# Optimization experiments

Measured on AMD Instinct MI355X. Metric: run time of the kernel, lower is better.

Reference implementation:

```python
import jax, jax.numpy as jnp
import numpy as np

N_NODES = 100000
N_EDGES = 1600000
D = 128
LN_EPS = 1e-5


def setup_inputs() -> dict:
    key = jax.random.key(0)
    ks = jax.random.split(key, 6)
    return {
        "x": jax.random.normal(ks[0], (N_NODES, D), dtype=jnp.float32),
        "edge_src": jax.random.randint(ks[1], (N_EDGES,), 0, N_NODES, dtype=jnp.int32),
        "edge_dst": jax.random.randint(ks[2], (N_EDGES,), 0, N_NODES, dtype=jnp.int32),
        "edge_val": jax.random.uniform(ks[3], (N_EDGES,), dtype=jnp.float32),
        "w1": jax.random.normal(ks[4], (D,), dtype=jnp.float32),
        "w2": jax.random.normal(ks[5], (D,), dtype=jnp.float32),
        "ln1_g": jnp.ones((D,), dtype=jnp.float32),
        "ln1_b": jnp.zeros((D,), dtype=jnp.float32),
        "ln2_g": jnp.ones((D,), dtype=jnp.float32),
        "ln2_b": jnp.zeros((D,), dtype=jnp.float32),
    }


def _layer_norm(x, g, b):
    mu = jnp.mean(x, axis=-1, keepdims=True)
    var = jnp.mean(jnp.square(x - mu), axis=-1, keepdims=True)
    return (x - mu) * jax.lax.rsqrt(var + LN_EPS) * g + b


def _gat_layer(x, w, src, dst, val, g, b):
    # diag transform: h = x * w  (elementwise over features)
    h = x * w
    # sparse adjacency aggregation: out[dst] += val * h[src]
    msg = val[:, None] * h[src]  # [E, D]
    out = jax.ops.segment_sum(msg, dst, num_segments=x.shape[0])
    return _layer_norm(out, g, b)


def reference(x, edge_src, edge_dst, edge_val, w1, w2, ln1_g, ln1_b, ln2_g, ln2_b):
    # layer 0 (followed by ReLU; dropout is identity in eval mode)
    h = _gat_layer(x, w1, edge_src, edge_dst, edge_val, ln1_g, ln1_b)
    h = jax.nn.relu(h)
    # layer 1 (last layer: no ReLU/dropout)
    out = _gat_layer(h, w2, edge_src, edge_dst, edge_val, ln2_g, ln2_b)
    return out
```

## Files before the change

### kernel.cpp

```cpp
#include <hip/hip_runtime.h>

typedef __fp16 half2_t __attribute__((ext_vector_type(2)));

#define D 128
#define LN_EPS 1e-5f
#define BUCKET_NODES 128
#define BUCKET_SHIFT 7
#define EDGE_CAP 4096
#define FUSE_THREADS 512
#define K2_EPT 32
#define GT 1024

__device__ inline unsigned pack_h2(float a, float b) {
    half2_t p = __builtin_amdgcn_cvt_pkrtz(a, b);
    return __builtin_bit_cast(unsigned, p);
}

__global__ __launch_bounds__(FUSE_THREADS)
void conv_fill_kernel(const float* __restrict__ x, unsigned int* __restrict__ xb,
                      int conv_items, int conv_blocks,
                      const int* __restrict__ src, const int* __restrict__ dst,
                      const float* __restrict__ val,
                      int* __restrict__ gcnt, uint2* __restrict__ edges,
                      int E, int nbuckets) {
    if ((int)blockIdx.x < conv_blocks) {
        int i4 = blockIdx.x * FUSE_THREADS + threadIdx.x;
        if (i4 < conv_items) {
            int node = i4 >> 4, f4 = (i4 & 15) << 2;
            float4 xA = *(const float4*)(x + (size_t)node * D + f4);
            float4 xB = *(const float4*)(x + (size_t)node * D + 64 + f4);
            uint4 pw;
            pw.x = pack_h2(xA.x, xB.x); pw.y = pack_h2(xA.y, xB.y);
            pw.z = pack_h2(xA.z, xB.z); pw.w = pack_h2(xA.w, xB.w);
            *(uint4*)(xb + (size_t)node * 64 + f4) = pw;
        }
        return;
    }
    __shared__ int lcnt[1024];
    __shared__ int lbase[1024];
    int fb = (int)blockIdx.x - conv_blocks;
    for (int i = threadIdx.x; i < nbuckets; i += FUSE_THREADS) lcnt[i] = 0;
    __syncthreads();

    int base = fb * (FUSE_THREADS * K2_EPT);
    unsigned int br[K2_EPT];
    #pragma unroll
    for (int r = 0; r < K2_EPT; ++r) {
        int e = base + r * FUSE_THREADS + threadIdx.x;
        if (e < E) {
            int d = dst[e];
            int b = d >> BUCKET_SHIFT;
            int rk = atomicAdd(&lcnt[b], 1);
            br[r] = ((unsigned)b << 21) | ((unsigned)(d & (BUCKET_NODES - 1)) << 14)
                  | (unsigned)rk;
        }
    }
    __syncthreads();
    for (int i = threadIdx.x; i < nbuckets; i += FUSE_THREADS) {
        int c = lcnt[i];
        lbase[i] = c ? atomicAdd(&gcnt[i], c) : 0;
    }
    __syncthreads();
    #pragma unroll
    for (int r = 0; r < K2_EPT; ++r) {
        int e = base + r * FUSE_THREADS + threadIdx.x;
        if (e < E) {
            unsigned u = br[r];
            int b    = (int)(u >> 21);
            int dstl = (int)((u >> 14) & 127u);
            int rk   = (int)(u & 16383u);
            int slot = lbase[b] + rk;
            if (slot < EDGE_CAP)
                edges[(size_t)b * EDGE_CAP + slot] =
                    make_uint2((unsigned)src[e] | ((unsigned)dstl << 20),
                               __float_as_uint(val[e]));
        }
    }
}

__global__ __launch_bounds__(GT, 8)
void gather_ln_kernel(const uint4* __restrict__ h4,
                      const int* __restrict__ gcnt,
                      const uint2* __restrict__ edges_g,
                      const float* __restrict__ w,
                      const float* __restrict__ g,
                      const float* __restrict__ bb,
                      float* __restrict__ out_f32,
                      unsigned int* __restrict__ out_h,
                      int N, int mode) {
    __shared__ uint2 eL[EDGE_CAP];
    __shared__ int hist[BUCKET_NODES];
    __shared__ int scanb[BUCKET_NODES];
    __shared__ int obase[BUCKET_NODES];

    int bkt = blockIdx.x;
    int tid = threadIdx.x;
    int cnt = min(gcnt[bkt], EDGE_CAP);
    const uint2* ep = edges_g + (size_t)bkt * EDGE_CAP;

    if (tid < BUCKET_NODES) hist[tid] = 0;
    __syncthreads();

    uint2 ed[4]; int dl[4]; int rk[4];
    #pragma unroll
    for (int r = 0; r < 4; ++r) {
        int i = r * GT + tid;
        if (i < cnt) {
            uint2 t = ep[i];
            ed[r] = t;
            dl[r] = (int)(t.x >> 20);
            rk[r] = atomicAdd(&hist[dl[r]], 1);
        } else dl[r] = -1;
    }
    __syncthreads();
    if (tid < BUCKET_NODES) scanb[tid] = hist[tid];
    __syncthreads();
    #pragma unroll
    for (int off = 1; off < BUCKET_NODES; off <<= 1) {
        int v = 0;
        if (tid < BUCKET_NODES && tid >= off) v = scanb[tid - off];
        __syncthreads();
        if (tid < BUCKET_NODES) scanb[tid] += v;
        __syncthreads();
    }
    if (tid < BUCKET_NODES) obase[tid] = scanb[tid] - hist[tid];
    __syncthreads();
    #pragma unroll
    for (int r = 0; r < 4; ++r)
        if (dl[r] >= 0) eL[obase[dl[r]] + rk[r]] = ed[r];
    __syncthreads();

    int wid = tid >> 6, lane = tid & 63, grp = lane >> 4, sl = lane & 15;

    float4 wA = ((const float4*)w)[sl];
    float4 wB = ((const float4*)(w + 64))[sl];
    float4 gA = ((const float4*)g)[sl];
    float4 gB = ((const float4*)(g + 64))[sl];
    float4 bA = ((const float4*)bb)[sl];
    float4 bB = ((const float4*)(bb + 64))[sl];

    #pragma unroll
    for (int k = 0; k < 2; ++k) {
        int ni = k * 64 + wid * 4 + grp;
        int n = (bkt << BUCKET_SHIFT) + ni;
        if (n >= N) continue;
        int st = obase[ni], m = hist[ni];

        float aA0=0,aA1=0,aA2=0,aA3=0, aB0=0,aB1=0,aB2=0,aB3=0;
        for (int j = 0; j < m; j += 2) {
            uint2 tA = eL[st + j];
            uint2 tB = (j + 1 < m) ? eL[st + j + 1] : make_uint2(0u, 0u);
            int   sA = (int)(tA.x & 0xfffffu);
            float vA = __uint_as_float(tA.y);
            int   sB = (int)(tB.x & 0xfffffu);
            float vB = __uint_as_float(tB.y);
            uint4 hA = h4[(size_t)sA * 16 + sl];
            uint4 hB = h4[(size_t)sB * 16 + sl];
            half2_t p;
            p = __builtin_bit_cast(half2_t, hA.x);
            aA0 = fmaf(vA, (float)p.x, aA0); aB0 = fmaf(vA, (float)p.y, aB0);
            p = __builtin_bit_cast(half2_t, hA.y);
            aA1 = fmaf(vA, (float)p.x, aA1); aB1 = fmaf(vA, (float)p.y, aB1);
            p = __builtin_bit_cast(half2_t, hA.z);
            aA2 = fmaf(vA, (float)p.x, aA2); aB2 = fmaf(vA, (float)p.y, aB2);
            p = __builtin_bit_cast(half2_t, hA.w);
            aA3 = fmaf(vA, (float)p.x, aA3); aB3 = fmaf(vA, (float)p.y, aB3);
            p = __builtin_bit_cast(half2_t, hB.x);
            aA0 = fmaf(vB, (float)p.x, aA0); aB0 = fmaf(vB, (float)p.y, aB0);
            p = __builtin_bit_cast(half2_t, hB.y);
            aA1 = fmaf(vB, (float)p.x, aA1); aB1 = fmaf(vB, (float)p.y, aB1);
            p = __builtin_bit_cast(half2_t, hB.z);
            aA2 = fmaf(vB, (float)p.x, aA2); aB2 = fmaf(vB, (float)p.y, aB2);
            p = __builtin_bit_cast(half2_t, hB.w);
            aA3 = fmaf(vB, (float)p.x, aA3); aB3 = fmaf(vB, (float)p.y, aB3);
        }

        aA0 *= wA.x; aA1 *= wA.y; aA2 *= wA.z; aA3 *= wA.w;
        aB0 *= wB.x; aB1 *= wB.y; aB2 *= wB.z; aB3 *= wB.w;

        float sum = ((aA0 + aA1) + (aA2 + aA3)) + ((aB0 + aB1) + (aB2 + aB3));
        sum += __shfl_xor(sum, 1, 64); sum += __shfl_xor(sum, 2, 64);
        sum += __shfl_xor(sum, 4, 64); sum += __shfl_xor(sum, 8, 64);
        float mu = sum * (1.0f / D);

        float dA0 = aA0 - mu, dA1 = aA1 - mu, dA2 = aA2 - mu, dA3 = aA3 - mu;
        float dB0 = aB0 - mu, dB1 = aB1 - mu, dB2 = aB2 - mu, dB3 = aB3 - mu;
        float sq = ((dA0*dA0 + dA1*dA1) + (dA2*dA2 + dA3*dA3))
                 + ((dB0*dB0 + dB1*dB1) + (dB2*dB2 + dB3*dB3));
        sq += __shfl_xor(sq, 1, 64); sq += __shfl_xor(sq, 2, 64);
        sq += __shfl_xor(sq, 4, 64); sq += __shfl_xor(sq, 8, 64);
        float rstd = rsqrtf(sq * (1.0f / D) + LN_EPS);

        float oA0 = dA0 * rstd * gA.x + bA.x, oA1 = dA1 * rstd * gA.y + bA.y;
        float oA2 = dA2 * rstd * gA.z + bA.z, oA3 = dA3 * rstd * gA.w + bA.w;
        float oB0 = dB0 * rstd * gB.x + bB.x, oB1 = dB1 * rstd * gB.y + bB.y;
        float oB2 = dB2 * rstd * gB.z + bB.z, oB3 = dB3 * rstd * gB.w + bB.w;

        if (mode == 1) {
            oA0 = fmaxf(oA0, 0.f); oA1 = fmaxf(oA1, 0.f);
            oA2 = fmaxf(oA2, 0.f); oA3 = fmaxf(oA3, 0.f);
            oB0 = fmaxf(oB0, 0.f); oB1 = fmaxf(oB1, 0.f);
            oB2 = fmaxf(oB2, 0.f); oB3 = fmaxf(oB3, 0.f);
            uint4 pw;
            pw.x = pack_h2(oA0, oB0); pw.y = pack_h2(oA1, oB1);
            pw.z = pack_h2(oA2, oB2); pw.w = pack_h2(oA3, oB3);
            ((uint4*)(out_h + (size_t)n * 64))[sl] = pw;
        } else {
            ((float4*)(out_f32 + (size_t)n * D))[sl]      = make_float4(oA0, oA1, oA2, oA3);
            ((float4*)(out_f32 + (size_t)n * D + 64))[sl] = make_float4(oB0, oB1, oB2, oB3);
        }
    }
}

extern "C" void kernel_launch(void* const* d_in, const int* in_sizes, int n_in,
                              void* d_out, int out_size, void* d_ws, size_t ws_size,
                              hipStream_t stream) {
    const float* x    = (const float*)d_in[0];
    const int*   esrc = (const int*)d_in[1];
    const int*   edst = (const int*)d_in[2];
    const float* eval_= (const float*)d_in[3];
    const float* w1   = (const float*)d_in[4];
    const float* w2   = (const float*)d_in[5];
    const float* g1   = (const float*)d_in[6];
    const float* b1   = (const float*)d_in[7];
    const float* g2   = (const float*)d_in[8];
    const float* b2   = (const float*)d_in[9];
    float* out = (float*)d_out;

    const int N = in_sizes[0] / D;
    const int E = in_sizes[1];
    const int nbuckets = (N + BUCKET_NODES - 1) >> BUCKET_SHIFT;

    unsigned int* xb    = (unsigned int*)d_ws;
    unsigned int* hb    = xb + (size_t)N * 64;
    uint2*        edges = (uint2*)(hb + (size_t)N * 64);
    int*          gcnt  = (int*)(edges + (size_t)nbuckets * EDGE_CAP);

    const int conv_items  = N * 16;
    const int conv_blocks = (conv_items + FUSE_THREADS - 1) / FUSE_THREADS;
    const int fill_blocks = (E + FUSE_THREADS * K2_EPT - 1) / (FUSE_THREADS * K2_EPT);

    (void)hipMemsetAsync(gcnt, 0, (size_t)nbuckets * sizeof(int), stream);
    conv_fill_kernel<<<conv_blocks + fill_blocks, FUSE_THREADS, 0, stream>>>(
        x, xb, conv_items, conv_blocks, esrc, edst, eval_, gcnt, edges, E, nbuckets);
    gather_ln_kernel<<<nbuckets, GT, 0, stream>>>((const uint4*)xb, gcnt, edges,
                                                  w1, g1, b1, nullptr, hb, N, 1);
    gather_ln_kernel<<<nbuckets, GT, 0, stream>>>((const uint4*)hb, gcnt, edges,
                                                  w2, g2, b2, out, nullptr, N, 0);
}
```

Before: 333.2 us.

## Split edge fill into more blocks and keep edge payload in registers

Cuts edges handled per thread in the bucketing fill from 32 to 4, launching many more fill blocks and placing them ahead of the fp16 conversion blocks. The src/val payload is loaded once during the counting pass and held in registers instead of being re-read after the global offset reservation. This raises parallelism and reduces the long serial per-block latency, at the cost of many more per-bucket global atomics on the shared counter array.

```diff
diff --git a/kernel.cpp b/kernel.cpp
--- a/kernel.cpp
+++ b/kernel.cpp
@@ -8,7 +8,7 @@
 #define BUCKET_SHIFT 7
 #define EDGE_CAP 4096
 #define FUSE_THREADS 512
-#define K2_EPT 32
+#define K2_EPT 4
 #define GT 1024
 
 __device__ inline unsigned pack_h2(float a, float b) {
@@ -18,13 +18,13 @@
 
 __global__ __launch_bounds__(FUSE_THREADS)
 void conv_fill_kernel(const float* __restrict__ x, unsigned int* __restrict__ xb,
-                      int conv_items, int conv_blocks,
+                      int conv_items, int fill_blocks,
                       const int* __restrict__ src, const int* __restrict__ dst,
                       const float* __restrict__ val,
                       int* __restrict__ gcnt, uint2* __restrict__ edges,
                       int E, int nbuckets) {
-    if ((int)blockIdx.x < conv_blocks) {
-        int i4 = blockIdx.x * FUSE_THREADS + threadIdx.x;
+    if ((int)blockIdx.x >= fill_blocks) {
+        int i4 = ((int)blockIdx.x - fill_blocks) * FUSE_THREADS + threadIdx.x;
         if (i4 < conv_items) {
             int node = i4 >> 4, f4 = (i4 & 15) << 2;
             float4 xA = *(const float4*)(x + (size_t)node * D + f4);
@@ -38,12 +38,14 @@
     }
     __shared__ int lcnt[1024];
     __shared__ int lbase[1024];
-    int fb = (int)blockIdx.x - conv_blocks;
+    int fb = (int)blockIdx.x;
     for (int i = threadIdx.x; i < nbuckets; i += FUSE_THREADS) lcnt[i] = 0;
     __syncthreads();
 
     int base = fb * (FUSE_THREADS * K2_EPT);
-    unsigned int br[K2_EPT];
+    unsigned int w0[K2_EPT];
+    float        w1[K2_EPT];
+    int          br[K2_EPT];
     #pragma unroll
     for (int r = 0; r < K2_EPT; ++r) {
         int e = base + r * FUSE_THREADS + threadIdx.x;
@@ -51,8 +53,11 @@
             int d = dst[e];
             int b = d >> BUCKET_SHIFT;
             int rk = atomicAdd(&lcnt[b], 1);
-            br[r] = ((unsigned)b << 21) | ((unsigned)(d & (BUCKET_NODES - 1)) << 14)
-                  | (unsigned)rk;
+            w0[r] = (unsigned)src[e] | ((unsigned)(d & (BUCKET_NODES - 1)) << 20);
+            w1[r] = val[e];
+            br[r] = (b << 16) | rk;
+        } else {
+            br[r] = -1;
         }
     }
     __syncthreads();
@@ -63,17 +68,13 @@
     __syncthreads();
     #pragma unroll
     for (int r = 0; r < K2_EPT; ++r) {
-        int e = base + r * FUSE_THREADS + threadIdx.x;
-        if (e < E) {
-            unsigned u = br[r];
-            int b    = (int)(u >> 21);
-            int dstl = (int)((u >> 14) & 127u);
-            int rk   = (int)(u & 16383u);
+        if (br[r] >= 0) {
+            int b    = br[r] >> 16;
+            int rk   = br[r] & 0xffff;
             int slot = lbase[b] + rk;
             if (slot < EDGE_CAP)
                 edges[(size_t)b * EDGE_CAP + slot] =
-                    make_uint2((unsigned)src[e] | ((unsigned)dstl << 20),
-                               __float_as_uint(val[e]));
+                    make_uint2(w0[r], __float_as_uint(w1[r]));
         }
     }
 }
@@ -241,8 +242,8 @@
     const int fill_blocks = (E + FUSE_THREADS * K2_EPT - 1) / (FUSE_THREADS * K2_EPT);
 
     (void)hipMemsetAsync(gcnt, 0, (size_t)nbuckets * sizeof(int), stream);
-    conv_fill_kernel<<<conv_blocks + fill_blocks, FUSE_THREADS, 0, stream>>>(
-        x, xb, conv_items, conv_blocks, esrc, edst, eval_, gcnt, edges, E, nbuckets);
+    conv_fill_kernel<<<fill_blocks + conv_blocks, FUSE_THREADS, 0, stream>>>(
+        x, xb, conv_items, fill_blocks, esrc, edst, eval_, gcnt, edges, E, nbuckets);
     gather_ln_kernel<<<nbuckets, GT, 0, stream>>>((const uint4*)xb, gcnt, edges,
                                                   w1, g1, b1, nullptr, hb, N, 1);
     gather_ln_kernel<<<nbuckets, GT, 0, stream>>>((const uint4*)hb, gcnt, edges,
```

Result: faster. 285.1 us (-14.4%).
